# Kernel tuning notes

Hardware: AMD Instinct MI355X
Metric: run time of the kernel (lower is better)

## Reference

```python
import jax, jax.numpy as jnp
import numpy as np
import math

# (mul, l, parity) triples for irreps_in1 == irreps_in2 == '32x0e+16x1o+8x2e'
IRREPS = [(32, 0, 1), (16, 1, -1), (8, 2, 1)]
BATCH = 2048


def _fact(n):
    return math.factorial(n)


def _w3j_entry(j1, j2, j3, m1, m2, m3):
    # Racah formula for the (complex-basis) Wigner 3j symbol, integer l's.
    if m1 + m2 + m3 != 0:
        return 0.0
    t_min = max(0, j2 - j3 - m1, j1 - j3 + m2)
    t_max = min(j1 + j2 - j3, j1 - m1, j2 + m2)
    if t_max < t_min:
        return 0.0
    s = 0.0
    for t in range(t_min, t_max + 1):
        s += (-1) ** t / (
            _fact(t) * _fact(j3 - j2 + t + m1) * _fact(j3 - j1 + t - m2)
            * _fact(j1 + j2 - j3 - t) * _fact(j1 - t - m1) * _fact(j2 - t + m2))
    delta = math.sqrt(_fact(j1 + j2 - j3) * _fact(j1 - j2 + j3)
                      * _fact(-j1 + j2 + j3) / _fact(j1 + j2 + j3 + 1))
    pref = math.sqrt(_fact(j1 + m1) * _fact(j1 - m1) * _fact(j2 + m2)
                     * _fact(j2 - m2) * _fact(j3 + m3) * _fact(j3 - m3))
    return (-1) ** (j1 - j2 - m3) * delta * pref * s


def _w3j_complex(j1, j2, j3):
    W = np.zeros((2 * j1 + 1, 2 * j2 + 1, 2 * j3 + 1))
    for m1 in range(-j1, j1 + 1):
        for m2 in range(-j2, j2 + 1):
            m3 = -(m1 + m2)
            if abs(m3) <= j3:
                W[m1 + j1, m2 + j2, m3 + j3] = _w3j_entry(j1, j2, j3, m1, m2, m3)
    return W


def _c2r(l):
    # complex -> real spherical harmonic change-of-basis (rows: real m, cols: complex mu)
    U = np.zeros((2 * l + 1, 2 * l + 1), dtype=np.complex128)
    U[l, l] = 1.0
    rs2 = 1.0 / math.sqrt(2.0)
    for m in range(1, l + 1):
        U[l + m, l + m] = (-1) ** m * rs2
        U[l + m, l - m] = rs2
        U[l - m, l - m] = 1j * rs2
        U[l - m, l + m] = -1j * (-1) ** m * rs2
    return U


def _w3j_real(l1, l2, l3):
    # Wigner 3j in the real spherical-harmonic basis (same sparsity/math as e3nn o3.wigner_3j)
    W = _w3j_complex(l1, l2, l3).astype(np.complex128)
    C = np.einsum('abc,ia,jb,kc->ijk', W, _c2r(l1), _c2r(l2), _c2r(l3))
    if np.linalg.norm(C.imag) > np.linalg.norm(C.real):
        C = np.ascontiguousarray(C.imag)
    else:
        C = np.ascontiguousarray(C.real)
    C[np.abs(C) < 1e-12] = 0.0
    return C


def _build_structure():
    # Mirrors CudaTensorProduct.__init__ with irreps_out=None: enumerate every
    # then emit sparse COO entries (in1_idx, in2_idx, out_idx, cb_val).
    entries_by_l3 = {}
    off1 = 0
    for mul1, l1, p1 in IRREPS:
        off2_base = 0
        for mul2, l2, p2 in IRREPS:
            for l3 in range(abs(l1 - l2), l1 + l2 + 1):
                p3 = (p1 * p2 + 1) // 2
                o1 = off1
                for _i in range(mul1):
                    o2 = off2_base
                    for _j in range(mul2):
                        entries_by_l3.setdefault((l3, p3), []).append((l1, l2, o1, o2))
                        o2 += 2 * l2 + 1
                    o1 += 2 * l1 + 1
            off2_base += (2 * l2 + 1) * mul2
        off1 += (2 * l1 + 1) * mul1

    l3s = sorted(entries_by_l3.keys(), key=lambda x: 2 * (x[0] + 1) + x[1])
    in1_idx, in2_idx, out_idx, cb_vals = [], [], [], []
    row = 0
    w3j_cache = {}
    for l3, p3 in l3s:
        for l1, l2, o1, o2 in entries_by_l3[(l3, p3)]:
            key = (l1, l2, l3)
            if key not in w3j_cache:
                w3j_cache[key] = _w3j_real(l1, l2, l3)
            C = w3j_cache[key]
            scale = math.sqrt(2 * l3 + 1)
            for m3 in range(2 * l3 + 1):
                for m2 in range(2 * l2 + 1):
                    for m1 in range(2 * l1 + 1):
                        v = C[m1, m2, m3]
                        if v == 0.0:
                            continue
                        in1_idx.append(m1 + o1)
                        in2_idx.append(m2 + o2)
                        out_idx.append(m3 + row)
                        cb_vals.append(float(v * scale))
            row += 2 * l3 + 1

    # palette/index encoding, as in the module (palette[0] == 0 is the filler slot)
    palette = sorted(set(cb_vals))
    palette.insert(0, 0.0)
    lut = {v: i for i, v in enumerate(palette)}
    cb_idx = [lut[v] for v in cb_vals]
    return (np.asarray(in1_idx, np.int32), np.asarray(in2_idx, np.int32),
            np.asarray(out_idx, np.int32), np.asarray(cb_idx, np.int32),
            np.asarray(palette, np.float32), row)


def setup_inputs() -> dict:
    key = jax.random.key(0)
    k1, k2 = jax.random.split(key)
    i1, i2, io, ic, pal, cb_height = _build_structure()
    dim = sum(m * (2 * l + 1) for m, l, _ in IRREPS)  # 120
    return {
        'in1': jax.random.normal(k1, (BATCH, dim), jnp.float32),
        'in2': jax.random.normal(k2, (BATCH, dim), jnp.float32),
        'cb_palette': jnp.asarray(pal),
        'in1_indices': jnp.asarray(i1),
        'in2_indices': jnp.asarray(i2),
        'out_indices': jnp.asarray(io),
        'cb_indices': jnp.asarray(ic),
        'cb_height': int(cb_height),
    }


def reference(in1, in2, cb_palette, in1_indices, in2_indices, out_indices, cb_indices, cb_height):
    # intermediate[b, o] = sum_k palette[cb_idx[k]] * in1[b, i1[k]] * in2[b, i2[k]]
    vals = cb_palette[cb_indices]                                   # [K]
    contrib = in1[:, in1_indices] * in2[:, in2_indices] * vals[None, :]  # [B, K]
    # scatter-accumulate along the sparse output rows
    out = jax.ops.segment_sum(contrib.T, out_indices, num_segments=cb_height).T  # [B, cb_height]
    return out
```

## Files before the change

kernel.cpp:

```cpp
#include <hip/hip_runtime.h>

#define DIM 120
#define NB 16
#define BLOCK 256

__global__ void row_ptr_kernel(const int* __restrict__ out_idx, int K, int H,
                               int* __restrict__ row_start) {
    int o = blockIdx.x * blockDim.x + threadIdx.x;
    if (o > H) return;
    int lo = 0, hi = K;
    while (lo < hi) {
        int mid = (lo + hi) >> 1;
        if (out_idx[mid] < o) lo = mid + 1; else hi = mid;
    }
    row_start[o] = lo;
}

__global__ void pack_kernel(const int* __restrict__ i1, const int* __restrict__ i2,
                            const int* __restrict__ cb, const float* __restrict__ pal,
                            int K, uint2* __restrict__ ent) {
    int k = blockIdx.x * blockDim.x + threadIdx.x;
    if (k >= K) return;
    uint2 e;
    e.x = (unsigned)i1[k] | ((unsigned)i2[k] << 16);
    e.y = __float_as_uint(pal[cb[k]]);
    ent[k] = e;
}

__global__ __launch_bounds__(BLOCK) void tp_kernel(
    const float* __restrict__ in1, const float* __restrict__ in2,
    const uint2* __restrict__ ent, const int* __restrict__ row_start,
    float* __restrict__ out, int H) {
    __shared__ float s1[NB * DIM];
    __shared__ float s2[NB * DIM];

    const int b0 = blockIdx.y * NB;
    {
        const float4* __restrict__ p1 = (const float4*)(in1 + (size_t)b0 * DIM);
        const float4* __restrict__ p2 = (const float4*)(in2 + (size_t)b0 * DIM);
        float4* q1 = (float4*)s1;
        float4* q2 = (float4*)s2;
        for (int t = threadIdx.x; t < NB * DIM / 4; t += BLOCK) {
            q1[t] = p1[t];
            q2[t] = p2[t];
        }
    }
    __syncthreads();

    const int o = blockIdx.x * BLOCK + threadIdx.x;
    if (o >= H) return;
    const int k0 = row_start[o];
    const int k1 = row_start[o + 1];

    float acc[NB];
#pragma unroll
    for (int b = 0; b < NB; ++b) acc[b] = 0.0f;

    for (int k = k0; k < k1; ++k) {
        const uint2 e = ent[k];
        const int a = e.x & 0xffff;
        const int c = e.x >> 16;
        const float v = __uint_as_float(e.y);
#pragma unroll
        for (int b = 0; b < NB; ++b)
            acc[b] += v * s1[b * DIM + a] * s2[b * DIM + c];
    }

#pragma unroll
    for (int b = 0; b < NB; ++b)
        out[(size_t)(b0 + b) * H + o] = acc[b];
}

extern "C" void kernel_launch(void* const* d_in, const int* in_sizes, int n_in,
                              void* d_out, int out_size, void* d_ws, size_t ws_size,
                              hipStream_t stream) {
    const float* in1 = (const float*)d_in[0];
    const float* in2 = (const float*)d_in[1];
    const float* pal = (const float*)d_in[2];
    const int*   i1  = (const int*)d_in[3];
    const int*   i2  = (const int*)d_in[4];
    const int*   oi  = (const int*)d_in[5];
    const int*   cb  = (const int*)d_in[6];

    const int K = in_sizes[3];
    const int B = in_sizes[0] / DIM;
    const int H = out_size / B;

    uint2* ent = (uint2*)d_ws;
    int* row_start = (int*)((char*)d_ws + (size_t)K * sizeof(uint2));

    row_ptr_kernel<<<(H + 1 + 255) / 256, 256, 0, stream>>>(oi, K, H, row_start);
    pack_kernel<<<(K + 255) / 256, 256, 0, stream>>>(i1, i2, cb, pal, K, ent);

    dim3 grid((H + BLOCK - 1) / BLOCK, B / NB);
    tp_kernel<<<grid, BLOCK, 0, stream>>>(in1, in2, ent, row_start,
                                          (float*)d_out, H);
}
```

Baseline: 35.27 us.

## Transpose shared inputs to batch-minor layout, double batch tile, fuse prep kernels

Shared-memory copies of in1/in2 are stored transposed (dim-major, batch-minor, padded to 36), so each sparse entry reads 32 batch values as contiguous float4 vectors instead of strided scalars. The batch tile per block grows from 16 to 32, so each entry fetch and index decode serves more outputs. The two preprocessing kernels are merged into one launch. The costs are a scattered transposing store into LDS with possible bank conflicts, twice the per-thread accumulators (more register pressure), and half as many blocks in the grid.

New measurement: 40.59 us. 1.15x slower.

```diff
diff --git a/kernel.cpp b/kernel.cpp
--- a/kernel.cpp
+++ b/kernel.cpp
@@ -1,48 +1,52 @@
 #include <hip/hip_runtime.h>
 
 #define DIM 120
-#define NB 16
+#define NB 32
+#define NBP 36
 #define BLOCK 256
 
-__global__ void row_ptr_kernel(const int* __restrict__ out_idx, int K, int H,
-                               int* __restrict__ row_start) {
-    int o = blockIdx.x * blockDim.x + threadIdx.x;
-    if (o > H) return;
-    int lo = 0, hi = K;
-    while (lo < hi) {
-        int mid = (lo + hi) >> 1;
-        if (out_idx[mid] < o) lo = mid + 1; else hi = mid;
+__global__ void pre_kernel(const int* __restrict__ out_idx, int K, int H,
+                           int* __restrict__ row_start,
+                           const int* __restrict__ i1, const int* __restrict__ i2,
+                           const int* __restrict__ cb, const float* __restrict__ pal,
+                           uint2* __restrict__ ent) {
+    int t = blockIdx.x * blockDim.x + threadIdx.x;
+    if (t <= H) {
+        int lo = 0, hi = K;
+        while (lo < hi) {
+            int mid = (lo + hi) >> 1;
+            if (out_idx[mid] < t) lo = mid + 1; else hi = mid;
+        }
+        row_start[t] = lo;
     }
-    row_start[o] = lo;
-}
-
-__global__ void pack_kernel(const int* __restrict__ i1, const int* __restrict__ i2,
-                            const int* __restrict__ cb, const float* __restrict__ pal,
-                            int K, uint2* __restrict__ ent) {
-    int k = blockIdx.x * blockDim.x + threadIdx.x;
-    if (k >= K) return;
-    uint2 e;
-    e.x = (unsigned)i1[k] | ((unsigned)i2[k] << 16);
-    e.y = __float_as_uint(pal[cb[k]]);
-    ent[k] = e;
+    if (t < K) {
+        uint2 e;
+        e.x = (unsigned)i1[t] | ((unsigned)i2[t] << 16);
+        e.y = __float_as_uint(pal[cb[t]]);
+        ent[t] = e;
+    }
 }
 
 __global__ __launch_bounds__(BLOCK) void tp_kernel(
     const float* __restrict__ in1, const float* __restrict__ in2,
     const uint2* __restrict__ ent, const int* __restrict__ row_start,
     float* __restrict__ out, int H) {
-    __shared__ float s1[NB * DIM];
-    __shared__ float s2[NB * DIM];
+    __shared__ float s1t[DIM * NBP];
+    __shared__ float s2t[DIM * NBP];
 
     const int b0 = blockIdx.y * NB;
     {
         const float4* __restrict__ p1 = (const float4*)(in1 + (size_t)b0 * DIM);
         const float4* __restrict__ p2 = (const float4*)(in2 + (size_t)b0 * DIM);
-        float4* q1 = (float4*)s1;
-        float4* q2 = (float4*)s2;
         for (int t = threadIdx.x; t < NB * DIM / 4; t += BLOCK) {
-            q1[t] = p1[t];
-            q2[t] = p2[t];
+            const int b  = t / (DIM / 4);
+            const int d  = (t % (DIM / 4)) * 4;
+            const float4 x = p1[t];
+            const float4 y = p2[t];
+            s1t[(d + 0) * NBP + b] = x.x; s1t[(d + 1) * NBP + b] = x.y;
+            s1t[(d + 2) * NBP + b] = x.z; s1t[(d + 3) * NBP + b] = x.w;
+            s2t[(d + 0) * NBP + b] = y.x; s2t[(d + 1) * NBP + b] = y.y;
+            s2t[(d + 2) * NBP + b] = y.z; s2t[(d + 3) * NBP + b] = y.w;
         }
     }
     __syncthreads();
@@ -58,12 +62,18 @@
 
     for (int k = k0; k < k1; ++k) {
         const uint2 e = ent[k];
-        const int a = e.x & 0xffff;
-        const int c = e.x >> 16;
+        const float4* __restrict__ pa = (const float4*)(s1t + (e.x & 0xffffu) * NBP);
+        const float4* __restrict__ pc = (const float4*)(s2t + (e.x >> 16) * NBP);
         const float v = __uint_as_float(e.y);
 #pragma unroll
-        for (int b = 0; b < NB; ++b)
-            acc[b] += v * s1[b * DIM + a] * s2[b * DIM + c];
+        for (int j = 0; j < NB / 4; ++j) {
+            const float4 x = pa[j];
+            const float4 y = pc[j];
+            acc[4 * j + 0] = fmaf(v * x.x, y.x, acc[4 * j + 0]);
+            acc[4 * j + 1] = fmaf(v * x.y, y.y, acc[4 * j + 1]);
+            acc[4 * j + 2] = fmaf(v * x.z, y.z, acc[4 * j + 2]);
+            acc[4 * j + 3] = fmaf(v * x.w, y.w, acc[4 * j + 3]);
+        }
     }
 
 #pragma unroll
@@ -89,8 +99,11 @@
     uint2* ent = (uint2*)d_ws;
     int* row_start = (int*)((char*)d_ws + (size_t)K * sizeof(uint2));
 
-    row_ptr_kernel<<<(H + 1 + 255) / 256, 256, 0, stream>>>(oi, K, H, row_start);
-    pack_kernel<<<(K + 255) / 256, 256, 0, stream>>>(i1, i2, cb, pal, K, ent);
+    {
+        const int n = (K > H + 1) ? K : (H + 1);
+        pre_kernel<<<(n + 255) / 256, 256, 0, stream>>>(oi, K, H, row_start,
+                                                        i1, i2, cb, pal, ent);
+    }
 
     dim3 grid((H + BLOCK - 1) / BLOCK, B / NB);
     tp_kernel<<<grid, BLOCK, 0, stream>>>(in1, in2, ent, row_start,
```
